# Kernel tuning notes

Hardware: AMD Instinct MI355X
Metric: run time of the kernel (lower is better)

## Reference

```python
import jax, jax.numpy as jnp
import numpy as np

THETA = 10000.0
R_TOK = 4  # region_token_num


def _local_positions(regions, max_n):
    # 0-based position of each token within its region (count of prior tokens
    # with the same region id) -- order-based, works for any region layout.
    onehot = jax.nn.one_hot(regions, max_n + 1, dtype=jnp.int32)  # [B,T,N+1]
    counts = jnp.cumsum(onehot, axis=1)                            # inclusive
    return jnp.take_along_axis(counts, regions[..., None], axis=-1)[..., 0] - 1


def _rope(q, k, pos, theta):
    # full-head-dim rotary embedding, split-half convention
    D = q.shape[-1]
    inv_freq = 1.0 / (theta ** (jnp.arange(0, D, 2, dtype=jnp.float32) / D))  # [D/2]
    ang = pos[..., None].astype(jnp.float32) * inv_freq                        # [B,S,D/2]
    cos = jnp.tile(jnp.cos(ang), (1, 1, 2))[:, None]                           # [B,1,S,D]
    sin = jnp.tile(jnp.sin(ang), (1, 1, 2))[:, None]

    def rot(x):
        h = x.shape[-1] // 2
        return jnp.concatenate([-x[..., h:], x[..., :h]], axis=-1)

    return q * cos + rot(q) * sin, k * cos + rot(k) * sin


def setup_inputs() -> dict:
    B, H, D = 2, 16, 64
    T, MAX_N = 2048, 64
    P = MAX_N * R_TOK
    key = jax.random.key(0)
    ks = jax.random.split(key, 7)
    f = lambda k, s: jax.random.normal(k, s, dtype=jnp.float32)
    regions = jnp.sort(jax.random.randint(ks[6], (B, T), 1, MAX_N + 1, dtype=jnp.int32), axis=-1)
    return {
        'pool_q': f(ks[0], (B, H, P, D)),
        'pool_k': f(ks[1], (B, H, P, D)),
        'pool_v': f(ks[2], (B, H, P, D)),
        'x_q': f(ks[3], (B, H, T, D)),
        'x_k': f(ks[4], (B, H, T, D)),
        'x_v': f(ks[5], (B, H, T, D)),
        'regions': regions,
        't_mask': jnp.ones((B, T), dtype=bool),
        'n_mask': jnp.ones((B, MAX_N), dtype=bool),
        'max_n': MAX_N,
    }


def reference(pool_q, pool_k, pool_v, x_q, x_k, x_v, regions, t_mask, n_mask, max_n):
    B, H, P, D = pool_q.shape
    R = R_TOK
    # sequence = [pool, x]
    q = jnp.concatenate([pool_q, x_q], axis=2)
    k = jnp.concatenate([pool_k, x_k], axis=2)
    v = jnp.concatenate([pool_v, x_v], axis=2)

    # local-mode positions (use_pool_offset=False -> pool tokens at pos 0)
    pool_pos = jnp.zeros((B, P), dtype=jnp.int32)
    x_pos = (_local_positions(regions, max_n) + R) * (regions > 0).astype(jnp.int32)
    pos = jnp.concatenate([pool_pos, x_pos], axis=-1)  # [B,S]
    q, k = _rope(q, k, pos, THETA)

    # block-local (same-region) mask: [B,1,S,S], True = allowed
    pool_region = jnp.broadcast_to(jnp.repeat(jnp.arange(1, max_n + 1, dtype=jnp.int32), R)[None], (B, P))
    pool_valid = jnp.repeat(n_mask, R, axis=1)                      # [B,P]
    full_region = jnp.concatenate([pool_region, regions], axis=-1)  # [B,S]
    full_valid = jnp.concatenate([pool_valid, t_mask], axis=-1)     # [B,S]
    same = full_region[:, :, None] == full_region[:, None, :]
    valid = full_valid[:, :, None] & full_valid[:, None, :]
    nonpad = (full_region != 0)[:, :, None] & (full_region != 0)[:, None, :]
    mask = (same & valid & nonpad)[:, None]                          # [B,1,S,S]

    scores = jnp.einsum('bhqd,bhkd->bhqk', q, k) / jnp.sqrt(jnp.float32(D))
    scores = jnp.where(mask, scores, jnp.float32(-1e9))
    attn = jax.nn.softmax(scores, axis=-1)
    out = jnp.einsum('bhqk,bhkd->bhqd', attn, v)
    return out[:, :, :P, :]
```

## Files before the change

kernel.cpp:

```cpp
#include <hip/hip_runtime.h>
#include <hip/hip_bf16.h>

#define BB   2
#define HH   16
#define DD   64
#define TT   2048
#define MAXN 64
#define RTOK 4
#define PP   (MAXN * RTOK)
#define PAD  68

__global__ __launch_bounds__(256)
void build_ranges(const int* __restrict__ regions, int* __restrict__ tab) {
    const int b   = blockIdx.x;
    const int tid = threadIdx.x;
    const int* reg = regions + b * TT;
    int* t = tab + b * 66;
    const int i0 = tid * 8;
    int v[9];
    const int4 a0 = *(const int4*)(reg + i0);
    const int4 a1 = *(const int4*)(reg + i0 + 4);
    v[0] = a0.x; v[1] = a0.y; v[2] = a0.z; v[3] = a0.w;
    v[4] = a1.x; v[5] = a1.y; v[6] = a1.z; v[7] = a1.w;
    v[8] = (tid == 255) ? (MAXN + 1) : reg[i0 + 8];
    if (tid == 0)
        for (int rr = 1; rr <= v[0]; ++rr) t[rr] = 0;
    #pragma unroll
    for (int j = 0; j < 8; ++j)
        for (int rr = v[j] + 1; rr <= v[j + 1]; ++rr) t[rr] = i0 + j + 1;
}

__device__ __forceinline__ void stage_x(const float* __restrict__ xk,
                                        const float* __restrict__ xv,
                                        int start, int xbase, int nx, int koff,
                                        int nrows, int tid,
                                        float (*k_s)[PAD], float (*v_t)[PAD]) {
    float4 kv[4], vv[4];
    int dim[4], xi_u[4];
    #pragma unroll
    for (int p = 0; p < 4; ++p) {
        const int flat = p * 1024 + tid * 4;
        xi_u[p] = flat >> 6;
        dim[p]  = flat & 63;
        const int xi = min(xi_u[p], nx - 1);
        const size_t off = (size_t)(start + xbase + xi) * DD;
        kv[p] = *(const float4*)(xk + off + dim[p]);
        vv[p] = *(const float4*)(xv + off + dim[p]);
    }
    #pragma unroll
    for (int p = 0; p < 4; ++p) {
        float4 kp;
        kp.x = __shfl_xor(kv[p].x, 8, 64);
        kp.y = __shfl_xor(kv[p].y, 8, 64);
        kp.z = __shfl_xor(kv[p].z, 8, 64);
        kp.w = __shfl_xor(kv[p].w, 8, 64);
        const int key = koff + xi_u[p];
        if (key < 64) {
            const int d = dim[p];
            const float pos = (float)(xbase + xi_u[p] + RTOK);
            const float sgn = (d < 32) ? -1.0f : 1.0f;
            const float kd[4]  = {kv[p].x, kv[p].y, kv[p].z, kv[p].w};
            const float kpd[4] = {kp.x, kp.y, kp.z, kp.w};
            float kr[4];
            #pragma unroll
            for (int c = 0; c < 4; ++c) {
                const int j = (d + c) & 31;
                const float invf = __expf((float)j * (-9.210340371976184f / 32.0f));
                float sv, cv;
                __sincosf(pos * invf, &sv, &cv);
                kr[c] = kd[c] * cv + sgn * kpd[c] * sv;
            }
            *(float4*)&k_s[key][d] = make_float4(kr[0], kr[1], kr[2], kr[3]);
            v_t[d + 0][key] = vv[p].x;
            v_t[d + 1][key] = vv[p].y;
            v_t[d + 2][key] = vv[p].z;
            v_t[d + 3][key] = vv[p].w;
        }
    }
}

__global__ __launch_bounds__(256, 4)
void lapd_attn(const float* __restrict__ pool_q,
               const float* __restrict__ pool_k,
               const float* __restrict__ pool_v,
               const float* __restrict__ x_k,
               const float* __restrict__ x_v,
               const int* __restrict__ tab,
               float* __restrict__ out) {
    const int blk   = blockIdx.x;
    const int r_idx = blk & (MAXN - 1);
    const int bh    = blk >> 6;
    const int b     = bh / HH;

    const int tid  = threadIdx.x;
    const int wave = tid >> 6;
    const int lane = tid & 63;

    __shared__ float k_s[64][PAD];
    __shared__ float v_t[64][PAD];
    __shared__ float q_s[4][DD];
    __shared__ float p_s[4][64];

    const int* tb   = tab + b * 66;
    const int start = tb[r_idx + 1];
    const int cnt   = tb[r_idx + 2] - start;

    const size_t poolbase = ((size_t)bh * PP + r_idx * RTOK) * DD;
    const float* pk = pool_k + poolbase;
    const float* pv = pool_v + poolbase;
    const float* xk = x_k + (size_t)bh * TT * DD;
    const float* xv = x_v + (size_t)bh * TT * DD;

    const size_t qidx = poolbase + (size_t)(wave * DD) + lane;
    const float qv = pool_q[qidx] * 0.125f;
    q_s[wave][lane] = qv;

    if (tid < 64) {
        const int key = tid >> 4, d = (tid & 15) * 4;
        const float4 kvp = *(const float4*)(pk + key * DD + d);
        const float4 vvp = *(const float4*)(pv + key * DD + d);
        *(float4*)&k_s[key][d] = kvp;
        v_t[d + 0][key] = vvp.x;
        v_t[d + 1][key] = vvp.y;
        v_t[d + 2][key] = vvp.z;
        v_t[d + 3][key] = vvp.w;
    }

    int tn, xbase;
    if (cnt > 0) {
        const int nx0 = min(cnt, 60);
        stage_x(xk, xv, start, 0, nx0, RTOK, 60, tid, k_s, v_t);
        tn = RTOK + nx0;
        xbase = nx0;
    } else {
        for (int i = tid; i < 60 * DD; i += 256) {
            const int key = 4 + (i >> 6), d = i & 63;
            k_s[key][d] = 0.0f;
            v_t[d][key] = 0.0f;
        }
        tn = RTOK;
        xbase = 0;
    }

    float m = -1e30f, l = 0.0f, acc = 0.0f;

    for (;;) {
        __syncthreads();

        float s = -1e30f;
        if (lane < tn) {
            float s0 = 0, s1 = 0, s2 = 0, s3 = 0;
            #pragma unroll
            for (int d = 0; d < DD; d += 4) {
                const float4 kk = *(const float4*)&k_s[lane][d];
                s0 += q_s[wave][d + 0] * kk.x;
                s1 += q_s[wave][d + 1] * kk.y;
                s2 += q_s[wave][d + 2] * kk.z;
                s3 += q_s[wave][d + 3] * kk.w;
            }
            s = (s0 + s1) + (s2 + s3);
        }
        float tm = s;
        #pragma unroll
        for (int off = 32; off > 0; off >>= 1)
            tm = fmaxf(tm, __shfl_xor(tm, off, 64));
        const float m_new = fmaxf(m, tm);
        const float alpha = __expf(m - m_new);
        const float p = (lane < tn) ? __expf(s - m_new) : 0.0f;
        float ts = p;
        #pragma unroll
        for (int off = 32; off > 0; off >>= 1)
            ts += __shfl_xor(ts, off, 64);
        l = l * alpha + ts;
        m = m_new;
        p_s[wave][lane] = p;

        acc *= alpha;
        float a0 = 0, a1 = 0, a2 = 0, a3 = 0;
        #pragma unroll
        for (int k = 0; k < 64; k += 4) {
            const float4 vv4 = *(const float4*)&v_t[lane][k];
            a0 += p_s[wave][k + 0] * vv4.x;
            a1 += p_s[wave][k + 1] * vv4.y;
            a2 += p_s[wave][k + 2] * vv4.z;
            a3 += p_s[wave][k + 3] * vv4.w;
        }
        acc += (a0 + a1) + (a2 + a3);

        if (xbase >= cnt) break;
        __syncthreads();
        const int nx = min(64, cnt - xbase);
        stage_x(xk, xv, start, xbase, nx, 0, 64, tid, k_s, v_t);
        tn = nx;
        xbase += nx;
    }

    out[qidx] = acc / l;
}

extern "C" void kernel_launch(void* const* d_in, const int* in_sizes, int n_in,
                              void* d_out, int out_size, void* d_ws, size_t ws_size,
                              hipStream_t stream) {
    const float* pool_q  = (const float*)d_in[0];
    const float* pool_k  = (const float*)d_in[1];
    const float* pool_v  = (const float*)d_in[2];
    const float* x_k     = (const float*)d_in[4];
    const float* x_v     = (const float*)d_in[5];
    const int*   regions = (const int*)d_in[6];
    float*       out     = (float*)d_out;
    int*         tab     = (int*)d_ws;

    build_ranges<<<dim3(BB), dim3(256), 0, stream>>>(regions, tab);
    lapd_attn<<<dim3(BB * HH * MAXN), dim3(256), 0, stream>>>(
        pool_q, pool_k, pool_v, x_k, x_v, tab, out);
}
```

Before: 114.4 us.

## Fuse RoPE and QK scores into staging, drop K shared tile and online max

K tiles are no longer written to shared memory. Each thread rotates its loaded K fragment, dots it against register-held Q slices for all four queries, and reduces the scores with lane shuffles. The online-softmax running max is removed: unnormalized exp(score) is written straight to p_s, and the row sum is accumulated inside the PV loop. This cuts LDS usage, which allows more blocks per CU (launch bounds raised to 6), and it precomputes the inverse frequencies once per thread. The trade-off is a risk of exp overflow if scores grow large, plus more shuffle traffic.

```diff
diff --git a/kernel.cpp b/kernel.cpp
--- a/kernel.cpp
+++ b/kernel.cpp
@@ -8,7 +8,7 @@
 #define MAXN 64
 #define RTOK 4
 #define PP   (MAXN * RTOK)
-#define PAD  68
+#define VPAD 68
 
 __global__ __launch_bounds__(256)
 void build_ranges(const int* __restrict__ regions, int* __restrict__ tab) {
@@ -30,56 +30,7 @@
         for (int rr = v[j] + 1; rr <= v[j + 1]; ++rr) t[rr] = i0 + j + 1;
 }
 
-__device__ __forceinline__ void stage_x(const float* __restrict__ xk,
-                                        const float* __restrict__ xv,
-                                        int start, int xbase, int nx, int koff,
-                                        int nrows, int tid,
-                                        float (*k_s)[PAD], float (*v_t)[PAD]) {
-    float4 kv[4], vv[4];
-    int dim[4], xi_u[4];
-    #pragma unroll
-    for (int p = 0; p < 4; ++p) {
-        const int flat = p * 1024 + tid * 4;
-        xi_u[p] = flat >> 6;
-        dim[p]  = flat & 63;
-        const int xi = min(xi_u[p], nx - 1);
-        const size_t off = (size_t)(start + xbase + xi) * DD;
-        kv[p] = *(const float4*)(xk + off + dim[p]);
-        vv[p] = *(const float4*)(xv + off + dim[p]);
-    }
-    #pragma unroll
-    for (int p = 0; p < 4; ++p) {
-        float4 kp;
-        kp.x = __shfl_xor(kv[p].x, 8, 64);
-        kp.y = __shfl_xor(kv[p].y, 8, 64);
-        kp.z = __shfl_xor(kv[p].z, 8, 64);
-        kp.w = __shfl_xor(kv[p].w, 8, 64);
-        const int key = koff + xi_u[p];
-        if (key < 64) {
-            const int d = dim[p];
-            const float pos = (float)(xbase + xi_u[p] + RTOK);
-            const float sgn = (d < 32) ? -1.0f : 1.0f;
-            const float kd[4]  = {kv[p].x, kv[p].y, kv[p].z, kv[p].w};
-            const float kpd[4] = {kp.x, kp.y, kp.z, kp.w};
-            float kr[4];
-            #pragma unroll
-            for (int c = 0; c < 4; ++c) {
-                const int j = (d + c) & 31;
-                const float invf = __expf((float)j * (-9.210340371976184f / 32.0f));
-                float sv, cv;
-                __sincosf(pos * invf, &sv, &cv);
-                kr[c] = kd[c] * cv + sgn * kpd[c] * sv;
-            }
-            *(float4*)&k_s[key][d] = make_float4(kr[0], kr[1], kr[2], kr[3]);
-            v_t[d + 0][key] = vv[p].x;
-            v_t[d + 1][key] = vv[p].y;
-            v_t[d + 2][key] = vv[p].z;
-            v_t[d + 3][key] = vv[p].w;
-        }
-    }
-}
-
-__global__ __launch_bounds__(256, 4)
+__global__ __launch_bounds__(256, 6)
 void lapd_attn(const float* __restrict__ pool_q,
                const float* __restrict__ pool_k,
                const float* __restrict__ pool_v,
@@ -96,14 +47,14 @@
     const int wave = tid >> 6;
     const int lane = tid & 63;
 
-    __shared__ float k_s[64][PAD];
-    __shared__ float v_t[64][PAD];
+    __shared__ float v_t[DD][VPAD];
     __shared__ float q_s[4][DD];
     __shared__ float p_s[4][64];
 
     const int* tb   = tab + b * 66;
     const int start = tb[r_idx + 1];
     const int cnt   = tb[r_idx + 2] - start;
+    const int sstart = (cnt > 0) ? start : 0;
 
     const size_t poolbase = ((size_t)bh * PP + r_idx * RTOK) * DD;
     const float* pk = pool_k + poolbase;
@@ -113,86 +64,122 @@
 
     const size_t qidx = poolbase + (size_t)(wave * DD) + lane;
     const float qv = pool_q[qidx] * 0.125f;
+
+    const int key0 = tid >> 4;
+    const int d    = (tid & 15) * 4;
+
+    float invf[4];
+    #pragma unroll
+    for (int c = 0; c < 4; ++c)
+        invf[c] = __expf((float)((d + c) & 31) * (-9.210340371976184f / 32.0f));
+    const float sgn = (d < 32) ? -1.0f : 1.0f;
+
     q_s[wave][lane] = qv;
-
-    if (tid < 64) {
-        const int key = tid >> 4, d = (tid & 15) * 4;
-        const float4 kvp = *(const float4*)(pk + key * DD + d);
-        const float4 vvp = *(const float4*)(pv + key * DD + d);
-        *(float4*)&k_s[key][d] = kvp;
-        v_t[d + 0][key] = vvp.x;
-        v_t[d + 1][key] = vvp.y;
-        v_t[d + 2][key] = vvp.z;
-        v_t[d + 3][key] = vvp.w;
-    }
-
-    int tn, xbase;
-    if (cnt > 0) {
-        const int nx0 = min(cnt, 60);
-        stage_x(xk, xv, start, 0, nx0, RTOK, 60, tid, k_s, v_t);
-        tn = RTOK + nx0;
-        xbase = nx0;
-    } else {
-        for (int i = tid; i < 60 * DD; i += 256) {
-            const int key = 4 + (i >> 6), d = i & 63;
-            k_s[key][d] = 0.0f;
-            v_t[d][key] = 0.0f;
+    __syncthreads();
+
+    float qr[4][4];
+    #pragma unroll
+    for (int w = 0; w < 4; ++w)
+        #pragma unroll
+        for (int c = 0; c < 4; ++c)
+            qr[w][c] = q_s[w][d + c];
+
+    float acc = 0.0f, l = 0.0f;
+    int xbase = 0;
+    bool first = true;
+
+    for (;;) {
+        const int koff = first ? RTOK : 0;
+        int nx = cnt - xbase;
+        if (nx > 64 - koff) nx = 64 - koff;
+        const int tn = koff + (nx > 0 ? nx : 0);
+
+        #pragma unroll
+        for (int half = 0; half < 2; ++half) {
+            float4 kv[2], vv[2];
+            int keyv[2], xiv[2];
+            #pragma unroll
+            for (int i = 0; i < 2; ++i) {
+                const int key = key0 + (half * 2 + i) * 16;
+                keyv[i] = key;
+                int xi = key - koff;
+                if (xi > nx - 1) xi = nx - 1;
+                if (xi < 0) xi = 0;
+                xiv[i] = xi;
+                if (first && key < RTOK) {
+                    kv[i] = *(const float4*)(pk + key * DD + d);
+                    vv[i] = *(const float4*)(pv + key * DD + d);
+                } else {
+                    const size_t off = (size_t)(sstart + xbase + xi) * DD;
+                    kv[i] = *(const float4*)(xk + off + d);
+                    vv[i] = *(const float4*)(xv + off + d);
+                }
+            }
+            #pragma unroll
+            for (int i = 0; i < 2; ++i) {
+                const int key = keyv[i];
+                float4 kp;
+                kp.x = __shfl_xor(kv[i].x, 8, 64);
+                kp.y = __shfl_xor(kv[i].y, 8, 64);
+                kp.z = __shfl_xor(kv[i].z, 8, 64);
+                kp.w = __shfl_xor(kv[i].w, 8, 64);
+                float kr[4] = {kv[i].x, kv[i].y, kv[i].z, kv[i].w};
+                if (!(first && key < RTOK)) {
+                    const float pos = (float)(xbase + xiv[i] + RTOK);
+                    const float kpd[4] = {kp.x, kp.y, kp.z, kp.w};
+                    #pragma unroll
+                    for (int c = 0; c < 4; ++c) {
+                        float sv, cv;
+                        __sincosf(pos * invf[c], &sv, &cv);
+                        kr[c] = kr[c] * cv + sgn * kpd[c] * sv;
+                    }
+                }
+                v_t[d + 0][key] = vv[i].x;
+                v_t[d + 1][key] = vv[i].y;
+                v_t[d + 2][key] = vv[i].z;
+                v_t[d + 3][key] = vv[i].w;
+                float s0 = qr[0][0]*kr[0] + qr[0][1]*kr[1] + qr[0][2]*kr[2] + qr[0][3]*kr[3];
+                float s1 = qr[1][0]*kr[0] + qr[1][1]*kr[1] + qr[1][2]*kr[2] + qr[1][3]*kr[3];
+                float s2 = qr[2][0]*kr[0] + qr[2][1]*kr[1] + qr[2][2]*kr[2] + qr[2][3]*kr[3];
+                float s3 = qr[3][0]*kr[0] + qr[3][1]*kr[1] + qr[3][2]*kr[2] + qr[3][3]*kr[3];
+                #pragma unroll
+                for (int off = 1; off <= 8; off <<= 1) {
+                    s0 += __shfl_xor(s0, off, 64);
+                    s1 += __shfl_xor(s1, off, 64);
+                    s2 += __shfl_xor(s2, off, 64);
+                    s3 += __shfl_xor(s3, off, 64);
+                }
+                const int sub = lane & 15;
+                if (sub < 4) {
+                    const float sq = (sub == 0) ? s0 : (sub == 1) ? s1
+                                   : (sub == 2) ? s2 : s3;
+                    p_s[sub][key] = (key < tn) ? __expf(sq) : 0.0f;
+                }
+            }
         }
-        tn = RTOK;
-        xbase = 0;
-    }
-
-    float m = -1e30f, l = 0.0f, acc = 0.0f;
-
-    for (;;) {
         __syncthreads();
 
-        float s = -1e30f;
-        if (lane < tn) {
-            float s0 = 0, s1 = 0, s2 = 0, s3 = 0;
-            #pragma unroll
-            for (int d = 0; d < DD; d += 4) {
-                const float4 kk = *(const float4*)&k_s[lane][d];
-                s0 += q_s[wave][d + 0] * kk.x;
-                s1 += q_s[wave][d + 1] * kk.y;
-                s2 += q_s[wave][d + 2] * kk.z;
-                s3 += q_s[wave][d + 3] * kk.w;
-            }
-            s = (s0 + s1) + (s2 + s3);
-        }
-        float tm = s;
-        #pragma unroll
-        for (int off = 32; off > 0; off >>= 1)
-            tm = fmaxf(tm, __shfl_xor(tm, off, 64));
-        const float m_new = fmaxf(m, tm);
-        const float alpha = __expf(m - m_new);
-        const float p = (lane < tn) ? __expf(s - m_new) : 0.0f;
-        float ts = p;
-        #pragma unroll
-        for (int off = 32; off > 0; off >>= 1)
-            ts += __shfl_xor(ts, off, 64);
-        l = l * alpha + ts;
-        m = m_new;
-        p_s[wave][lane] = p;
-
-        acc *= alpha;
-        float a0 = 0, a1 = 0, a2 = 0, a3 = 0;
+        float a0 = 0, a1 = 0, a2 = 0, a3 = 0, l0 = 0;
         #pragma unroll
         for (int k = 0; k < 64; k += 4) {
-            const float4 vv4 = *(const float4*)&v_t[lane][k];
-            a0 += p_s[wave][k + 0] * vv4.x;
-            a1 += p_s[wave][k + 1] * vv4.y;
-            a2 += p_s[wave][k + 2] * vv4.z;
-            a3 += p_s[wave][k + 3] * vv4.w;
+            const float4 v4 = *(const float4*)&v_t[lane][k];
+            const float p0 = p_s[wave][k + 0];
+            const float p1 = p_s[wave][k + 1];
+            const float p2 = p_s[wave][k + 2];
+            const float p3 = p_s[wave][k + 3];
+            a0 += p0 * v4.x;
+            a1 += p1 * v4.y;
+            a2 += p2 * v4.z;
+            a3 += p3 * v4.w;
+            l0 += (p0 + p1) + (p2 + p3);
         }
         acc += (a0 + a1) + (a2 + a3);
-
+        l   += l0;
+
+        xbase += (nx > 0 ? nx : 0);
+        first = false;
         if (xbase >= cnt) break;
         __syncthreads();
-        const int nx = min(64, cnt - xbase);
-        stage_x(xk, xv, start, xbase, nx, 0, 64, tid, k_s, v_t);
-        tn = nx;
-        xbase += nx;
     }
 
     out[qidx] = acc / l;
```

Result: slower. 124.1 us (+8.5%).
